# Kernel optimization log

Measured on AMD Instinct MI355X. Metric: run time of the kernel, lower is better.

The kernel has to match this reference:

```python
import jax, jax.numpy as jnp
import numpy as np

K = 128          # num_clusters (init kwarg k)
N_ITERS = 100    # torch loop runs up to 100 iters; converged centroids are a
                 # fixed point, so running all 100 matches the early-exit result


def _sq_dists(x, c):
    # squared Euclidean distances [N, K]; argmin identical to torch.cdist argmin
    return (jnp.sum(x * x, axis=1, keepdims=True)
            - 2.0 * (x @ c.T)
            + jnp.sum(c * c, axis=1)[None, :])


def _assign_and_update(x, c):
    ids = jnp.argmin(_sq_dists(x, c), axis=1)                     # [N]
    sums = jax.ops.segment_sum(x, ids, num_segments=K)            # [K, D]
    counts = jax.ops.segment_sum(jnp.ones((x.shape[0],), x.dtype), ids,
                                 num_segments=K)                  # [K]
    return ids, sums / counts[:, None]   # mean per cluster (NaN if empty, as in torch)


def setup_inputs() -> dict:
    key = jax.random.key(0)
    kx, kp = jax.random.split(key)
    N, D = 32768, 256
    x = jax.random.normal(kx, (N, D), dtype=jnp.float32)
    # torch.randperm(N)[:K] -> distinct initial centroid indices
    init_idx = jax.random.permutation(kp, N)[:K].astype(jnp.int32)
    return {"x": x, "init_idx": init_idx}


def reference(x, init_idx):
    c0 = x[init_idx]  # [K, D]

    def body(c, _):
        _, newc = _assign_and_update(x, c)
        return newc, None

    # 99 updates, then final assignment + update: returned ids correspond to the
    # centroids BEFORE the last update, exactly like the torch loop's last iter.
    c, _ = jax.lax.scan(body, c0, None, length=N_ITERS - 1)
    ids, c = _assign_and_update(x, c)

    logits = x @ c.T  # temperature = 1.0
    logp = jax.nn.log_softmax(logits, axis=-1)
    # CrossEntropyLoss(mean) with pseudo labels = cluster ids
    loss = -jnp.mean(jnp.take_along_axis(logp, ids[:, None], axis=1))
    return loss
```

## Files before the change

kernel.cpp:

```cpp
#include <hip/hip_runtime.h>
#include <cstdint>

#define NPTS 32768
#define DIM  256
#define NK   128
#define NITER 100
#define NBLK 256
#define NTHR 512
#define PAD  33

typedef unsigned short ushort_t;
typedef __attribute__((ext_vector_type(8))) short s8v;
typedef __attribute__((ext_vector_type(4))) float f4v;

__device__ __forceinline__ unsigned short f2bf(float f) {
  unsigned u = __float_as_uint(f);
  u += 0x7fffu + ((u >> 16) & 1u);
  return (unsigned short)(u >> 16);
}
__device__ __forceinline__ float bf2f(unsigned short b) {
  return __uint_as_float(((unsigned)b) << 16);
}

__device__ __forceinline__ void cstore(float* p, float v) {
  __hip_atomic_store(p, v, __ATOMIC_RELAXED, __HIP_MEMORY_SCOPE_AGENT);
}
__device__ __forceinline__ float cload(const float* p) {
  return __hip_atomic_load(p, __ATOMIC_RELAXED, __HIP_MEMORY_SCOPE_AGENT);
}
__device__ __forceinline__ void cstorei(int* p, int v) {
  __hip_atomic_store(p, v, __ATOMIC_RELAXED, __HIP_MEMORY_SCOPE_AGENT);
}
__device__ __forceinline__ int cloadi(const int* p) {
  return __hip_atomic_load(p, __ATOMIC_RELAXED, __HIP_MEMORY_SCOPE_AGENT);
}

__device__ __forceinline__ void stage4(const ushort_t* __restrict__ src, s8v* buf, int h, int t) {
  const int lane = t & 63;
  const int wb = (t >> 6) << 6;
#pragma unroll
  for (int i = 0; i < 4; ++i) {
    const int Gb = i * 512 + wb;
    const int G  = Gb + lane;
    const int Gs = G ^ ((G >> 4) & 7);
    const char* ga = (const char*)src + (G >> 4) * 512 + h * 256 + (Gs & 15) * 16;
    __builtin_amdgcn_global_load_lds(
        (const __attribute__((address_space(1))) void*)ga,
        (__attribute__((address_space(3))) void*)((char*)buf + Gb * 16),
        16, 0, 0);
  }
}

__device__ __forceinline__ void gbar_core(unsigned* flags, unsigned* ggen, unsigned gen, bool fence) {
  if (blockIdx.x == 0) {
    const int t = threadIdx.x;
    if (t >= 1 && t < NBLK) {
      while (__hip_atomic_load(&flags[t * 16], __ATOMIC_RELAXED, __HIP_MEMORY_SCOPE_AGENT) < gen)
        __builtin_amdgcn_s_sleep(1);
    }
    __syncthreads();
    if (t == 0) {
      if (fence) __threadfence();
      __hip_atomic_store(ggen, gen, __ATOMIC_RELEASE, __HIP_MEMORY_SCOPE_AGENT);
    }
  } else {
    if (threadIdx.x == 0) {
      if (fence) __threadfence();
      __hip_atomic_store(&flags[blockIdx.x * 16], gen, __ATOMIC_RELEASE, __HIP_MEMORY_SCOPE_AGENT);
      while (__hip_atomic_load(ggen, __ATOMIC_RELAXED, __HIP_MEMORY_SCOPE_AGENT) < gen)
        __builtin_amdgcn_s_sleep(1);
      if (fence) __threadfence();
    }
  }
  asm volatile("" ::: "memory");
  __syncthreads();
}

__device__ __forceinline__ void gbar_nf(unsigned* flags, unsigned* ggen, unsigned gen) {
  __syncthreads();
  gbar_core(flags, ggen, gen, false);
}
__device__ __forceinline__ void gbar_f(unsigned* flags, unsigned* ggen, unsigned gen) {
  __syncthreads();
  gbar_core(flags, ggen, gen, true);
}
__device__ __forceinline__ void gbar_f_pf(unsigned* flags, unsigned* ggen, unsigned gen,
    const ushort_t* xhb, const ushort_t* xlb, s8v (*bufs)[2048], int t) {
  __syncthreads();
  stage4(xhb, bufs[0], 0, t);
  stage4(xlb, bufs[1], 0, t);
  gbar_core(flags, ggen, gen, true);
}

struct SMa {
  s8v bufs[4][2048];
  float cns[NK];
  float redd[NK * 4];
  int   redk[NK * 4];
  float gmaxs[NK];
  float labvs[NK];
  int   labis[NK];
};

__device__ __forceinline__ void gemm_core(
    SMa& sm, int t,
    const ushort_t* __restrict__ xhb, const ushort_t* __restrict__ xlb,
    const ushort_t* __restrict__ chi, const ushort_t* __restrict__ clo,
    const float* __restrict__ cn, f4v (&acc)[4][2]) {
  const int lane = t & 63;
  const int w    = t >> 6;
  const int wr   = w >> 2, wc = w & 3;
  const int g    = lane >> 4, lr = lane & 15;

  if (t < NK) sm.cns[t] = cn[t];

  const f4v zero = {0.f, 0.f, 0.f, 0.f};
#pragma unroll
  for (int i = 0; i < 4; ++i)
#pragma unroll
    for (int j = 0; j < 2; ++j) acc[i][j] = zero;

  const int swz = (lr & 7) << 4;
  int a_off[4], b_off[2];
#pragma unroll
  for (int i = 0; i < 4; ++i) a_off[i] = (wr * 64 + i * 16 + lr) * 256 + g * 16;
#pragma unroll
  for (int j = 0; j < 2; ++j) b_off[j] = (wc * 32 + j * 16 + lr) * 256 + g * 16;

  for (int h = 0; h < 2; ++h) {
    stage4(chi, sm.bufs[2], h, t);
    stage4(clo, sm.bufs[3], h, t);
    if (h == 1) {
      stage4(xhb, sm.bufs[0], h, t);
      stage4(xlb, sm.bufs[1], h, t);
    }
    __syncthreads();
#pragma unroll
    for (int kk = 0; kk < 4; ++kk) {
      s8v ah[4], al[4], bh[2], bl[2];
#pragma unroll
      for (int i = 0; i < 4; ++i) {
        int o = (a_off[i] + kk * 64) ^ swz;
        ah[i] = *(const s8v*)((const char*)sm.bufs[0] + o);
        al[i] = *(const s8v*)((const char*)sm.bufs[1] + o);
      }
#pragma unroll
      for (int j = 0; j < 2; ++j) {
        int o = (b_off[j] + kk * 64) ^ swz;
        bh[j] = *(const s8v*)((const char*)sm.bufs[2] + o);
        bl[j] = *(const s8v*)((const char*)sm.bufs[3] + o);
      }
#pragma unroll
      for (int i = 0; i < 4; ++i)
#pragma unroll
        for (int j = 0; j < 2; ++j) {
          acc[i][j] = __builtin_amdgcn_mfma_f32_16x16x32_bf16(ah[i], bh[j], acc[i][j], 0, 0, 0);
          acc[i][j] = __builtin_amdgcn_mfma_f32_16x16x32_bf16(ah[i], bl[j], acc[i][j], 0, 0, 0);
          acc[i][j] = __builtin_amdgcn_mfma_f32_16x16x32_bf16(al[i], bh[j], acc[i][j], 0, 0, 0);
        }
    }
    if (h == 0) __syncthreads();
  }
}

__global__ __launch_bounds__(NTHR, 1) void kmeans_fused(
    const float* __restrict__ x, const int* __restrict__ init_idx,
    ushort_t* __restrict__ xh, ushort_t* __restrict__ xl,
    ushort_t* __restrict__ chi, ushort_t* __restrict__ clo,
    float* __restrict__ cn, int* __restrict__ ids,
    float* __restrict__ psum, float* __restrict__ pcnt,
    float* __restrict__ outp, unsigned* __restrict__ flags,
    unsigned* __restrict__ ggen, float* __restrict__ out) {
  __shared__ SMa sm;
  __shared__ float accB[NK * PAD];
  __shared__ int   idslB[1024];
  __shared__ int   cntB[NK];
  __shared__ float redsm[NTHR];

  const int b = blockIdx.x;
  const int t = threadIdx.x;
  const int lane = t & 63;
  const int w  = t >> 6;
  const int wr = w >> 2, wc = w & 3;
  const int g  = lane >> 4, lr = lane & 15;
  const int pbase = b * 128;
  const ushort_t* xhb = xh + (size_t)pbase * DIM;
  const ushort_t* xlb = xl + (size_t)pbase * DIM;
  unsigned gen = 1;

  for (int i = 0; i < 8; ++i) {
    int gg = b * 4096 + i * NTHR + t;
    const float4* src = (const float4*)x + gg * 2;
    float4 fa = src[0], fb = src[1];
    float vv[8] = {fa.x, fa.y, fa.z, fa.w, fb.x, fb.y, fb.z, fb.w};
    s8v vh, vl;
#pragma unroll
    for (int j = 0; j < 8; ++j) {
      unsigned short hh = f2bf(vv[j]);
      vh[j] = (short)hh;
      vl[j] = (short)f2bf(vv[j] - bf2f(hh));
    }
    ((s8v*)xh)[gg] = vh;
    ((s8v*)xl)[gg] = vl;
  }

  if (b < NK) {
    float eff = 0.f;
    if (t < DIM) {
      float v = x[init_idx[b] * DIM + t];
      unsigned short hh = f2bf(v);
      unsigned short ll = f2bf(v - bf2f(hh));
      chi[b * DIM + t] = hh;
      clo[b * DIM + t] = ll;
      eff = bf2f(hh) + bf2f(ll);
    }
    redsm[t] = eff * eff;
    __syncthreads();
    for (int s = 256; s > 0; s >>= 1) { if (t < s) redsm[t] += redsm[t + s]; __syncthreads(); }
    if (t == 0) cn[b] = redsm[0];
  }
  gbar_f_pf(flags, ggen, gen, xhb, xlb, sm.bufs, t); ++gen;

  for (int it = 0; it < NITER; ++it) {
    {
      f4v acc[4][2];
      gemm_core(sm, t, xhb, xlb, chi, clo, cn, acc);
#pragma unroll
      for (int i = 0; i < 4; ++i) {
#pragma unroll
        for (int r = 0; r < 4; ++r) {
          int prow = wr * 64 + i * 16 + g * 4 + r;
          float bd = 1e30f; int bk = 0;
#pragma unroll
          for (int j = 0; j < 2; ++j) {
            int col = wc * 32 + j * 16 + lr;
            float s = sm.cns[col] - 2.f * acc[i][j][r];
            if (s < bd || (s == bd && col < bk)) { bd = s; bk = col; }
          }
#pragma unroll
          for (int msk = 1; msk < 16; msk <<= 1) {
            float od = __shfl_xor(bd, msk, 64);
            int   ok = __shfl_xor(bk, msk, 64);
            if (od < bd || (od == bd && ok < bk)) { bd = od; bk = ok; }
          }
          if (lr == 0) { sm.redd[prow * 4 + wc] = bd; sm.redk[prow * 4 + wc] = bk; }
        }
      }
      __syncthreads();
      if (t < NK) {
        float bd = sm.redd[t * 4]; int bk = sm.redk[t * 4];
#pragma unroll
        for (int q = 1; q < 4; ++q) {
          float dq = sm.redd[t * 4 + q]; int kq = sm.redk[t * 4 + q];
          if (dq < bd || (dq == bd && kq < bk)) { bd = dq; bk = kq; }
        }
        cstorei(&ids[pbase + t], bk);
      }
    }
    gbar_nf(flags, ggen, gen); ++gen;

    {
      const int pg = b & 31, dg = b >> 5;
      for (int i = t; i < NK * PAD; i += NTHR) accB[i] = 0.f;
      if (t < NK) cntB[t] = 0;
      idslB[t]        = cloadi(&ids[pg * 1024 + t]);
      idslB[NTHR + t] = cloadi(&ids[pg * 1024 + NTHR + t]);
      __syncthreads();
      if (dg == 0) {
        atomicAdd(&cntB[idslB[t]], 1);
        atomicAdd(&cntB[idslB[NTHR + t]], 1);
      }
      const int qd = t & 7, ps = t >> 3;
      const float* xs = x + (size_t)pg * 1024 * DIM + dg * 32 + qd * 4;
#pragma unroll
      for (int s = 0; s < 16; ++s) {
        int pl = s * 64 + ps;
        int id = idslB[pl];
        float4 v = *(const float4*)(xs + (size_t)pl * DIM);
        atomicAdd(&accB[id * PAD + qd * 4 + 0], v.x);
        atomicAdd(&accB[id * PAD + qd * 4 + 1], v.y);
        atomicAdd(&accB[id * PAD + qd * 4 + 2], v.z);
        atomicAdd(&accB[id * PAD + qd * 4 + 3], v.w);
      }
      __syncthreads();
      const int kl = t >> 5, dl = t & 31;
#pragma unroll
      for (int s2 = 0; s2 < 8; ++s2) {
        int k2 = s2 * 16 + kl;
        cstore(&psum[(((size_t)dg * NK + k2) * 32 + pg) * 32 + dl], accB[k2 * PAD + dl]);
      }
      if (dg == 0 && t < NK)
        cstore(&pcnt[(size_t)pg * NK + t], (float)cntB[t]);
    }
    gbar_nf(flags, ggen, gen); ++gen;

    if (b < NK) {
      const int k = b;
      const int tt = t & 255, hf = t >> 8;
      const int dgc = tt >> 5, dlc = tt & 31;
      float s = 0.f;
#pragma unroll
      for (int p2 = hf * 16; p2 < hf * 16 + 16; ++p2)
        s += cload(&psum[(((size_t)dgc * NK + k) * 32 + p2) * 32 + dlc]);
      redsm[t] = s;
      float cv = 0.f;
      if (t < 32) cv = cload(&pcnt[(size_t)t * NK + k]);
      if (t < 64) {
#pragma unroll
        for (int m = 1; m < 32; m <<= 1) cv += __shfl_xor(cv, m, 64);
      }
      if (t == 0) sm.labvs[0] = cv;
      __syncthreads();
      if (t < DIM) {
        float cnt = sm.labvs[0];
        float mean = (redsm[t] + redsm[t + 256]) / cnt;
        unsigned short hh = f2bf(mean);
        unsigned short ll = f2bf(mean - bf2f(hh));
        chi[k * DIM + t] = hh;
        clo[k * DIM + t] = ll;
        float eff = bf2f(hh) + bf2f(ll);
        __syncthreads();
        redsm[t] = eff * eff;
      } else {
        __syncthreads();
        redsm[t] = 0.f;
      }
      __syncthreads();
      for (int st = 256; st > 0; st >>= 1) { if (t < st) redsm[t] += redsm[t + st]; __syncthreads(); }
      if (t == 0) cn[k] = redsm[0];
    }
    gbar_f_pf(flags, ggen, gen, xhb, xlb, sm.bufs, t); ++gen;
  }

  {
    f4v acc[4][2];
    gemm_core(sm, t, xhb, xlb, chi, clo, cn, acc);
#pragma unroll
    for (int i = 0; i < 4; ++i) {
#pragma unroll
      for (int r = 0; r < 4; ++r) {
        int prow = wr * 64 + i * 16 + g * 4 + r;
        float m = -1e30f;
#pragma unroll
        for (int j = 0; j < 2; ++j) m = fmaxf(m, acc[i][j][r]);
#pragma unroll
        for (int msk = 1; msk < 16; msk <<= 1) m = fmaxf(m, __shfl_xor(m, msk, 64));
        if (lr == 0) sm.redd[prow * 4 + wc] = m;
      }
    }
    __syncthreads();
    if (t < NK) {
      float m = sm.redd[t * 4];
#pragma unroll
      for (int q = 1; q < 4; ++q) m = fmaxf(m, sm.redd[t * 4 + q]);
      sm.gmaxs[t] = m;
      sm.labis[t] = cloadi(&ids[pbase + t]);
    }
    __syncthreads();
#pragma unroll
    for (int i = 0; i < 4; ++i) {
#pragma unroll
      for (int r = 0; r < 4; ++r) {
        int prow = wr * 64 + i * 16 + g * 4 + r;
        float m = sm.gmaxs[prow];
        int lab = sm.labis[prow];
        float s = 0.f;
#pragma unroll
        for (int j = 0; j < 2; ++j) {
          int col = wc * 32 + j * 16 + lr;
          float v = acc[i][j][r];
          s += expf(v - m);
          if (col == lab) sm.labvs[prow] = v;
        }
#pragma unroll
        for (int msk = 1; msk < 16; msk <<= 1) s += __shfl_xor(s, msk, 64);
        if (lr == 0) sm.redd[prow * 4 + wc] = s;
      }
    }
    __syncthreads();
    if (t < NK) {
      float se = sm.redd[t * 4] + sm.redd[t * 4 + 1] + sm.redd[t * 4 + 2] + sm.redd[t * 4 + 3];
      float lse = sm.gmaxs[t] + logf(se);
      sm.gmaxs[t] = lse - sm.labvs[t];
    }
    __syncthreads();
    if (t == 0) {
      float tot = 0.f;
      for (int q = 0; q < NK; ++q) tot += sm.gmaxs[q];
      outp[b] = tot;
    }
  }
  gbar_f(flags, ggen, gen); ++gen;
  if (b == 0) {
    redsm[t] = (t < NBLK) ? outp[t] : 0.f;
    __syncthreads();
    for (int s = 256; s > 0; s >>= 1) { if (t < s) redsm[t] += redsm[t + s]; __syncthreads(); }
    if (t == 0) out[0] = redsm[0] * (1.0f / (float)NPTS);
  }
}

extern "C" void kernel_launch(void* const* d_in, const int* in_sizes, int n_in,
                              void* d_out, int out_size, void* d_ws, size_t ws_size,
                              hipStream_t stream) {
  const float* x        = (const float*)d_in[0];
  const int*   init_idx = (const int*)d_in[1];
  float* out = (float*)d_out;
  char* ws = (char*)d_ws;

  ushort_t* xh  = (ushort_t*)(ws);
  ushort_t* xl  = (ushort_t*)(ws + 16777216);
  ushort_t* chi = (ushort_t*)(ws + 33554432);
  ushort_t* clo = (ushort_t*)(ws + 33619968);
  float* cn   = (float*)(ws + 33685504);
  int*   ids  = (int*)(ws + 33686016);
  float* psum = (float*)(ws + 33817088);
  float* pcnt = (float*)(ws + 67371520);
  float* outp = (float*)(ws + 67502592);
  unsigned* flags = (unsigned*)(ws + 67503616);
  unsigned* ggen  = (unsigned*)(ws + 67520000);

  hipMemsetAsync(flags, 0, 16448, stream);
  kmeans_fused<<<dim3(NBLK), dim3(NTHR), 0, stream>>>(
      x, init_idx, xh, xl, chi, clo, cn, ids, psum, pcnt, outp, flags, ggen, out);
}
```

Before: 8.486 ms.

## Replace master-block grid barrier with all-to-all flag barrier and packed coherent centroids

```diff
diff --git a/kernel.cpp b/kernel.cpp
--- a/kernel.cpp
+++ b/kernel.cpp
@@ -10,6 +10,7 @@
 #define PAD  33
 
 typedef unsigned short ushort_t;
+typedef unsigned long long ull_t;
 typedef __attribute__((ext_vector_type(8))) short s8v;
 typedef __attribute__((ext_vector_type(4))) float f4v;
 
@@ -32,6 +33,12 @@
   __hip_atomic_store(p, v, __ATOMIC_RELAXED, __HIP_MEMORY_SCOPE_AGENT);
 }
 __device__ __forceinline__ int cloadi(const int* p) {
+  return __hip_atomic_load(p, __ATOMIC_RELAXED, __HIP_MEMORY_SCOPE_AGENT);
+}
+__device__ __forceinline__ void cstore64(ull_t* p, ull_t v) {
+  __hip_atomic_store(p, v, __ATOMIC_RELAXED, __HIP_MEMORY_SCOPE_AGENT);
+}
+__device__ __forceinline__ ull_t cload64(const ull_t* p) {
   return __hip_atomic_load(p, __ATOMIC_RELAXED, __HIP_MEMORY_SCOPE_AGENT);
 }
 
@@ -51,45 +58,50 @@
   }
 }
 
-__device__ __forceinline__ void gbar_core(unsigned* flags, unsigned* ggen, unsigned gen, bool fence) {
-  if (blockIdx.x == 0) {
-    const int t = threadIdx.x;
-    if (t >= 1 && t < NBLK) {
-      while (__hip_atomic_load(&flags[t * 16], __ATOMIC_RELAXED, __HIP_MEMORY_SCOPE_AGENT) < gen)
-        __builtin_amdgcn_s_sleep(1);
-    }
-    __syncthreads();
-    if (t == 0) {
-      if (fence) __threadfence();
-      __hip_atomic_store(ggen, gen, __ATOMIC_RELEASE, __HIP_MEMORY_SCOPE_AGENT);
-    }
-  } else {
-    if (threadIdx.x == 0) {
-      if (fence) __threadfence();
-      __hip_atomic_store(&flags[blockIdx.x * 16], gen, __ATOMIC_RELEASE, __HIP_MEMORY_SCOPE_AGENT);
-      while (__hip_atomic_load(ggen, __ATOMIC_RELAXED, __HIP_MEMORY_SCOPE_AGENT) < gen)
-        __builtin_amdgcn_s_sleep(1);
-      if (fence) __threadfence();
-    }
+__device__ __forceinline__ void stage_c(const ull_t* __restrict__ cpk,
+                                        s8v* bh, s8v* bl, int h, int t) {
+#pragma unroll
+  for (int i = 0; i < 4; ++i) {
+    const int G = i * NTHR + t;
+    const int k = G >> 4, gcol = G & 15;
+    const int sc = gcol ^ (k & 7);
+    const ull_t* src = cpk + (size_t)k * 128 + h * 64 + sc * 4;
+    ull_t w0 = cload64(src + 0), w1 = cload64(src + 1);
+    ull_t w2 = cload64(src + 2), w3 = cload64(src + 3);
+    s8v vh, vl;
+    vh[0] = (short)w0; vl[0] = (short)(w0 >> 16); vh[1] = (short)(w0 >> 32); vl[1] = (short)(w0 >> 48);
+    vh[2] = (short)w1; vl[2] = (short)(w1 >> 16); vh[3] = (short)(w1 >> 32); vl[3] = (short)(w1 >> 48);
+    vh[4] = (short)w2; vl[4] = (short)(w2 >> 16); vh[5] = (short)(w2 >> 32); vl[5] = (short)(w2 >> 48);
+    vh[6] = (short)w3; vl[6] = (short)(w3 >> 16); vh[7] = (short)(w3 >> 32); vl[7] = (short)(w3 >> 48);
+    *(s8v*)((char*)bh + G * 16) = vh;
+    *(s8v*)((char*)bl + G * 16) = vl;
+  }
+}
+
+__device__ __forceinline__ void gbar(unsigned* flags, unsigned gen) {
+  __syncthreads();
+  if (threadIdx.x == 0)
+    __hip_atomic_store(&flags[blockIdx.x * 16], gen, __ATOMIC_RELAXED, __HIP_MEMORY_SCOPE_AGENT);
+  if (threadIdx.x < NBLK) {
+    while (__hip_atomic_load(&flags[threadIdx.x * 16], __ATOMIC_RELAXED, __HIP_MEMORY_SCOPE_AGENT) < gen)
+      __builtin_amdgcn_s_sleep(1);
   }
   asm volatile("" ::: "memory");
   __syncthreads();
 }
-
-__device__ __forceinline__ void gbar_nf(unsigned* flags, unsigned* ggen, unsigned gen) {
-  __syncthreads();
-  gbar_core(flags, ggen, gen, false);
-}
-__device__ __forceinline__ void gbar_f(unsigned* flags, unsigned* ggen, unsigned gen) {
-  __syncthreads();
-  gbar_core(flags, ggen, gen, true);
-}
-__device__ __forceinline__ void gbar_f_pf(unsigned* flags, unsigned* ggen, unsigned gen,
+__device__ __forceinline__ void gbar_pf(unsigned* flags, unsigned gen,
     const ushort_t* xhb, const ushort_t* xlb, s8v (*bufs)[2048], int t) {
   __syncthreads();
   stage4(xhb, bufs[0], 0, t);
   stage4(xlb, bufs[1], 0, t);
-  gbar_core(flags, ggen, gen, true);
+  if (t == 0)
+    __hip_atomic_store(&flags[blockIdx.x * 16], gen, __ATOMIC_RELAXED, __HIP_MEMORY_SCOPE_AGENT);
+  if (t < NBLK) {
+    while (__hip_atomic_load(&flags[t * 16], __ATOMIC_RELAXED, __HIP_MEMORY_SCOPE_AGENT) < gen)
+      __builtin_amdgcn_s_sleep(1);
+  }
+  asm volatile("" ::: "memory");
+  __syncthreads();
 }
 
 struct SMa {
@@ -105,14 +117,13 @@
 __device__ __forceinline__ void gemm_core(
     SMa& sm, int t,
     const ushort_t* __restrict__ xhb, const ushort_t* __restrict__ xlb,
-    const ushort_t* __restrict__ chi, const ushort_t* __restrict__ clo,
-    const float* __restrict__ cn, f4v (&acc)[4][2]) {
+    const ull_t* __restrict__ cpk, const float* __restrict__ cn, f4v (&acc)[4][2]) {
   const int lane = t & 63;
   const int w    = t >> 6;
   const int wr   = w >> 2, wc = w & 3;
   const int g    = lane >> 4, lr = lane & 15;
 
-  if (t < NK) sm.cns[t] = cn[t];
+  if (t < NK) sm.cns[t] = cload(&cn[t]);
 
   const f4v zero = {0.f, 0.f, 0.f, 0.f};
 #pragma unroll
@@ -128,12 +139,11 @@
   for (int j = 0; j < 2; ++j) b_off[j] = (wc * 32 + j * 16 + lr) * 256 + g * 16;
 
   for (int h = 0; h < 2; ++h) {
-    stage4(chi, sm.bufs[2], h, t);
-    stage4(clo, sm.bufs[3], h, t);
     if (h == 1) {
-      stage4(xhb, sm.bufs[0], h, t);
-      stage4(xlb, sm.bufs[1], h, t);
-    }
+      stage4(xhb, sm.bufs[0], 1, t);
+      stage4(xlb, sm.bufs[1], 1, t);
+    }
+    stage_c(cpk, sm.bufs[2], sm.bufs[3], h, t);
     __syncthreads();
 #pragma unroll
     for (int kk = 0; kk < 4; ++kk) {
@@ -166,16 +176,17 @@
 __global__ __launch_bounds__(NTHR, 1) void kmeans_fused(
     const float* __restrict__ x, const int* __restrict__ init_idx,
     ushort_t* __restrict__ xh, ushort_t* __restrict__ xl,
-    ushort_t* __restrict__ chi, ushort_t* __restrict__ clo,
-    float* __restrict__ cn, int* __restrict__ ids,
+    ull_t* __restrict__ cpk, float* __restrict__ cn, int* __restrict__ ids,
     float* __restrict__ psum, float* __restrict__ pcnt,
     float* __restrict__ outp, unsigned* __restrict__ flags,
-    unsigned* __restrict__ ggen, float* __restrict__ out) {
+    float* __restrict__ out) {
   __shared__ SMa sm;
   __shared__ float accB[NK * PAD];
   __shared__ int   idslB[1024];
   __shared__ int   cntB[NK];
   __shared__ float redsm[NTHR];
+  __shared__ ushort_t hsm[DIM], lsm[DIM];
+  __shared__ float cntsh;
 
   const int b = blockIdx.x;
   const int t = threadIdx.x;
@@ -210,21 +221,26 @@
       float v = x[init_idx[b] * DIM + t];
       unsigned short hh = f2bf(v);
       unsigned short ll = f2bf(v - bf2f(hh));
-      chi[b * DIM + t] = hh;
-      clo[b * DIM + t] = ll;
+      hsm[t] = hh; lsm[t] = ll;
       eff = bf2f(hh) + bf2f(ll);
     }
+    __syncthreads();
     redsm[t] = eff * eff;
+    if (t < NK) {
+      ull_t wv = (ull_t)hsm[2 * t] | ((ull_t)lsm[2 * t] << 16)
+               | ((ull_t)hsm[2 * t + 1] << 32) | ((ull_t)lsm[2 * t + 1] << 48);
+      cstore64(&cpk[(size_t)b * 128 + t], wv);
+    }
     __syncthreads();
     for (int s = 256; s > 0; s >>= 1) { if (t < s) redsm[t] += redsm[t + s]; __syncthreads(); }
-    if (t == 0) cn[b] = redsm[0];
-  }
-  gbar_f_pf(flags, ggen, gen, xhb, xlb, sm.bufs, t); ++gen;
+    if (t == 0) cstore(&cn[b], redsm[0]);
+  }
+  gbar_pf(flags, gen, xhb, xlb, sm.bufs, t); ++gen;
 
   for (int it = 0; it < NITER; ++it) {
     {
       f4v acc[4][2];
-      gemm_core(sm, t, xhb, xlb, chi, clo, cn, acc);
+      gemm_core(sm, t, xhb, xlb, cpk, cn, acc);
 #pragma unroll
       for (int i = 0; i < 4; ++i) {
 #pragma unroll
@@ -257,7 +273,7 @@
         cstorei(&ids[pbase + t], bk);
       }
     }
-    gbar_nf(flags, ggen, gen); ++gen;
+    gbar(flags, gen); ++gen;
 
     {
       const int pg = b & 31, dg = b >> 5;
@@ -292,7 +308,7 @@
       if (dg == 0 && t < NK)
         cstore(&pcnt[(size_t)pg * NK + t], (float)cntB[t]);
     }
-    gbar_nf(flags, ggen, gen); ++gen;
+    gbar(flags, gen); ++gen;
 
     if (b < NK) {
       const int k = b;
@@ -309,32 +325,33 @@
 #pragma unroll
         for (int m = 1; m < 32; m <<= 1) cv += __shfl_xor(cv, m, 64);
       }
-      if (t == 0) sm.labvs[0] = cv;
-      __syncthreads();
+      if (t == 0) cntsh = cv;
+      __syncthreads();
+      float eff = 0.f;
       if (t < DIM) {
-        float cnt = sm.labvs[0];
-        float mean = (redsm[t] + redsm[t + 256]) / cnt;
+        float mean = (redsm[t] + redsm[t + 256]) / cntsh;
         unsigned short hh = f2bf(mean);
         unsigned short ll = f2bf(mean - bf2f(hh));
-        chi[k * DIM + t] = hh;
-        clo[k * DIM + t] = ll;
-        float eff = bf2f(hh) + bf2f(ll);
-        __syncthreads();
-        redsm[t] = eff * eff;
-      } else {
-        __syncthreads();
-        redsm[t] = 0.f;
+        hsm[t] = hh; lsm[t] = ll;
+        eff = bf2f(hh) + bf2f(ll);
+      }
+      __syncthreads();
+      redsm[t] = eff * eff;
+      if (t < NK) {
+        ull_t wv = (ull_t)hsm[2 * t] | ((ull_t)lsm[2 * t] << 16)
+                 | ((ull_t)hsm[2 * t + 1] << 32) | ((ull_t)lsm[2 * t + 1] << 48);
+        cstore64(&cpk[(size_t)k * 128 + t], wv);
       }
       __syncthreads();
       for (int st = 256; st > 0; st >>= 1) { if (t < st) redsm[t] += redsm[t + st]; __syncthreads(); }
-      if (t == 0) cn[k] = redsm[0];
-    }
-    gbar_f_pf(flags, ggen, gen, xhb, xlb, sm.bufs, t); ++gen;
+      if (t == 0) cstore(&cn[k], redsm[0]);
+    }
+    gbar_pf(flags, gen, xhb, xlb, sm.bufs, t); ++gen;
   }
 
   {
     f4v acc[4][2];
-    gemm_core(sm, t, xhb, xlb, chi, clo, cn, acc);
+    gemm_core(sm, t, xhb, xlb, cpk, cn, acc);
 #pragma unroll
     for (int i = 0; i < 4; ++i) {
 #pragma unroll
@@ -387,12 +404,12 @@
     if (t == 0) {
       float tot = 0.f;
       for (int q = 0; q < NK; ++q) tot += sm.gmaxs[q];
-      outp[b] = tot;
-    }
-  }
-  gbar_f(flags, ggen, gen); ++gen;
+      cstore(&outp[b], tot);
+    }
+  }
+  gbar(flags, gen); ++gen;
   if (b == 0) {
-    redsm[t] = (t < NBLK) ? outp[t] : 0.f;
+    redsm[t] = (t < NBLK) ? cload(&outp[t]) : 0.f;
     __syncthreads();
     for (int s = 256; s > 0; s >>= 1) { if (t < s) redsm[t] += redsm[t + s]; __syncthreads(); }
     if (t == 0) out[0] = redsm[0] * (1.0f / (float)NPTS);
@@ -409,17 +426,15 @@
 
   ushort_t* xh  = (ushort_t*)(ws);
   ushort_t* xl  = (ushort_t*)(ws + 16777216);
-  ushort_t* chi = (ushort_t*)(ws + 33554432);
-  ushort_t* clo = (ushort_t*)(ws + 33619968);
+  ull_t* cpk  = (ull_t*)(ws + 33554432);
   float* cn   = (float*)(ws + 33685504);
   int*   ids  = (int*)(ws + 33686016);
   float* psum = (float*)(ws + 33817088);
-  float* pcnt = (float*)(ws + 67371520);
-  float* outp = (float*)(ws + 67502592);
-  unsigned* flags = (unsigned*)(ws + 67503616);
-  unsigned* ggen  = (unsigned*)(ws + 67520000);
-
-  hipMemsetAsync(flags, 0, 16448, stream);
+  float* pcnt = (float*)(ws + 38011392);
+  float* outp = (float*)(ws + 38027776);
+  unsigned* flags = (unsigned*)(ws + 38028800);
+
+  hipMemsetAsync(flags, 0, 16384, stream);
   kmeans_fused<<<dim3(NBLK), dim3(NTHR), 0, stream>>>(
-      x, init_idx, xh, xl, chi, clo, cn, ids, psum, pcnt, outp, flags, ggen, out);
-}
+      x, init_idx, xh, xl, cpk, cn, ids, psum, pcnt, outp, flags, out);
+}
```

Measured after the change: 6.976 ms. 1.22x faster.
